# Optimization experiments

Measured on AMD Instinct MI355X. Metric: run time of the kernel, lower is better.

Reference implementation:

```python
import jax, jax.numpy as jnp
import numpy as np

B, S, LEN = 1024, 64, 48          # batch, max atoms, atoms per molecule
N = B * LEN                        # total nodes = node_mask.sum()
E = 4 * N                          # edges (avg degree ~4)
D = 256                            # input_dim == hidden_dim == d_model == d_ff
H, HD = D // 8, 8                  # num_heads = hidden_dim // 8
L = 3                              # transformer layers
VOCAB = 65


def _ln(z, s, b):
    mu = z.mean(-1, keepdims=True)
    var = ((z - mu) ** 2).mean(-1, keepdims=True)
    return (z - mu) * jax.lax.rsqrt(var + 1e-5) * s + b


def _forward(x_atoms, edge_index, node_mask, emb_table, conv1_w, conv1_b,
             conv2_w, conv2_b, in_w, in_b, attn_w, attn_b, proj_w, proj_b,
             ln1_s, ln1_b, ff1_w, ff1_b, ff2_w, ff2_b, ln2_s, ln2_b):
    n = x_atoms.shape[0]
    src, dst = edge_index[0], edge_index[1]
    # Embedding with max_norm=1 (torch renormalizes accessed rows)
    e = emb_table[x_atoms]
    nrm = jnp.linalg.norm(e, axis=-1, keepdims=True)
    e = e * jnp.minimum(1.0, 1.0 / (nrm + 1e-7))
    # GCN symmetric normalization with self-loops (shared by both convs)
    deg = jax.ops.segment_sum(jnp.ones((src.shape[0],), e.dtype), dst, num_segments=n) + 1.0
    dinv = jax.lax.rsqrt(deg)
    coef = (dinv[src] * dinv[dst])[:, None]       # per-edge norm
    self_coef = (dinv * dinv)[:, None]            # self-loop norm

    def gcn(h, W, b):
        h = h @ W
        agg = jax.ops.segment_sum(h[src] * coef, dst, num_segments=n)
        return agg + h * self_coef + b

    ones = jnp.ones((n, 1), e.dtype)
    pe = jax.nn.relu(gcn(ones, conv1_w, conv1_b))
    pe = gcn(pe, conv2_w, conv2_b)
    x = e + pe
    # masked_scatter into padded [B, S, D] (row-major fill order)
    mflat = node_mask.reshape(-1)
    rank = jnp.clip(jnp.cumsum(mflat) - 1, 0, n - 1)
    padded = jnp.where(mflat[:, None], x[rank], 0.0).reshape(B, S, D)
    # transformer encoder, post-LN, ReLU FFN; mask [B,1,S,1] as in original
    h = padded @ in_w + in_b
    qmask = node_mask[:, None, :, None]
    scale = 1.0 / np.sqrt(HD).astype(np.float32)
    for l in range(L):
        qkv = h @ attn_w[l] + attn_b[l]
        q, k, v = jnp.split(qkv, 3, axis=-1)
        q = q.reshape(B, S, H, HD)
        k = k.reshape(B, S, H, HD)
        v = v.reshape(B, S, H, HD)
        scores = jnp.einsum('bqhd,bkhd->bhqk', q, k) * scale
        scores = jnp.where(qmask, scores, -1e9)
        attn = jax.nn.softmax(scores, axis=-1)
        o = jnp.einsum('bhqk,bkhd->bqhd', attn, v).reshape(B, S, D)
        h = _ln(h + o @ proj_w[l] + proj_b[l], ln1_s[l], ln1_b[l])
        ff = jax.nn.relu(h @ ff1_w[l] + ff1_b[l]) @ ff2_w[l] + ff2_b[l]
        h = _ln(h + ff, ln2_s[l], ln2_b[l])
    return h


def setup_inputs() -> dict:
    key = jax.random.key(0)
    ks = jax.random.split(key, 16)
    x_atoms = jax.random.randint(ks[0], (N,), 0, VOCAB)
    edge_index = jax.random.randint(ks[1], (2, E), 0, N)
    node_mask = jnp.broadcast_to(jnp.arange(S)[None, :] < LEN, (B, S))
    f32 = jnp.float32
    p = lambda k, shp: (jax.random.normal(k, shp, f32) * 0.02)
    return {
        'x_atoms': x_atoms, 'edge_index': edge_index, 'node_mask': node_mask,
        'emb_table': jax.random.normal(ks[2], (VOCAB, D), f32),
        'conv1_w': p(ks[3], (1, D)), 'conv1_b': jnp.zeros((D,), f32),
        'conv2_w': p(ks[4], (D, D)), 'conv2_b': jnp.zeros((D,), f32),
        'in_w': p(ks[5], (D, D)), 'in_b': jnp.zeros((D,), f32),
        'attn_w': p(ks[6], (L, D, 3 * D)), 'attn_b': jnp.zeros((L, 3 * D), f32),
        'proj_w': p(ks[7], (L, D, D)), 'proj_b': jnp.zeros((L, D), f32),
        'ln1_s': jnp.ones((L, D), f32), 'ln1_b': jnp.zeros((L, D), f32),
        'ff1_w': p(ks[8], (L, D, D)), 'ff1_b': jnp.zeros((L, D), f32),
        'ff2_w': p(ks[9], (L, D, D)), 'ff2_b': jnp.zeros((L, D), f32),
        'ln2_s': jnp.ones((L, D), f32), 'ln2_b': jnp.zeros((L, D), f32),
    }


def reference(x_atoms, edge_index, node_mask, emb_table, conv1_w, conv1_b,
              conv2_w, conv2_b, in_w, in_b, attn_w, attn_b, proj_w, proj_b,
              ln1_s, ln1_b, ff1_w, ff1_b, ff2_w, ff2_b, ln2_s, ln2_b):
    return _forward(x_atoms, edge_index, node_mask, emb_table, conv1_w, conv1_b,
                    conv2_w, conv2_b, in_w, in_b, attn_w, attn_b, proj_w, proj_b,
                    ln1_s, ln1_b, ff1_w, ff1_b, ff2_w, ff2_b, ln2_s, ln2_b)
```

## Files before the change

### kernel.cpp

```cpp
#include <hip/hip_runtime.h>
#include <cstdint>
#include <cstddef>

#define B_   1024
#define S_   64
#define LEN_ 48
#define NN   (B_*LEN_)
#define EE   (4*NN)
#define D_   256
#define H_   32
#define HD_  8
#define ROWS (B_*S_)
#define PLANE 16777216

typedef float  f32x4  __attribute__((ext_vector_type(4)));
typedef __bf16 bf16x8 __attribute__((ext_vector_type(8)));

#define AS1(p) ((const __attribute__((address_space(1))) void*)(p))
#define AS3(p) ((__attribute__((address_space(3))) void*)(p))

__device__ __forceinline__ unsigned short f2bf(float f) {
    union { float f; unsigned u; } x; x.f = f;
    unsigned r = x.u + 0x7fffu + ((x.u >> 16) & 1u);
    return (unsigned short)(r >> 16);
}
__device__ __forceinline__ float bf2f(unsigned short h) {
    union { unsigned u; float f; } x; x.u = (unsigned)h << 16; return x.f;
}
__device__ __forceinline__ bf16x8 u4_to_bf8(uint4 u) {
    union { uint4 u; bf16x8 v; } c; c.u = u; return c.v;
}

__global__ void embed_kernel(const int* __restrict__ atoms,
                             const float* __restrict__ table,
                             float* __restrict__ e) {
    int wave = threadIdx.x >> 6, lane = threadIdx.x & 63;
    int row  = blockIdx.x * 4 + wave;
    int a    = atoms[row];
    float4 v = ((const float4*)(table + (size_t)a * D_))[lane];
    float ss = v.x*v.x + v.y*v.y + v.z*v.z + v.w*v.w;
    #pragma unroll
    for (int off = 32; off; off >>= 1) ss += __shfl_xor(ss, off);
    float nrm = sqrtf(ss);
    float sc  = fminf(1.0f, 1.0f / (nrm + 1e-7f));
    v.x *= sc; v.y *= sc; v.z *= sc; v.w *= sc;
    ((float4*)(e + (size_t)row * D_))[lane] = v;
}

__global__ void fill_kernel(const int* __restrict__ ei, int* __restrict__ cur,
                            int* __restrict__ bucket) {
    int e = blockIdx.x * 256 + threadIdx.x;
    if (e < EE) {
        int s = ei[e], d = ei[EE + e];
        int pos = atomicAdd(&cur[d], 1);
        if (pos < 32) bucket[d * 32 + pos] = s;
    }
}

__global__ void dinv_kernel(const int* __restrict__ cur, float* __restrict__ dinv) {
    int i = blockIdx.x * 256 + threadIdx.x;
    if (i < NN) dinv[i] = rsqrtf((float)cur[i] + 1.0f);
}

__global__ void agg1_kernel(const int* __restrict__ ei, const float* __restrict__ dinv,
                            float* __restrict__ agg1) {
    int e = blockIdx.x * 256 + threadIdx.x;
    if (e < EE) {
        int s = ei[e], d = ei[EE + e];
        atomicAdd(&agg1[d], dinv[s] * dinv[d]);
    }
}

__global__ void pe1_kernel(const float* __restrict__ agg1, const float* __restrict__ dinv,
                           const float* __restrict__ w1, const float* __restrict__ b1,
                           unsigned short* __restrict__ pe1) {
    size_t idx = (size_t)blockIdx.x * 256 + threadIdx.x;
    int i = (int)(idx >> 8), d = (int)(idx & 255);
    float c = agg1[i] + dinv[i] * dinv[i];
    pe1[idx] = f2bf(fmaxf(0.0f, w1[d] * c + b1[d]));
}

__global__ void wconv_kernel(const float* __restrict__ conv2_w, const float* __restrict__ in_w,
                             const float* __restrict__ attn_w, const float* __restrict__ proj_w,
                             const float* __restrict__ ff1_w, const float* __restrict__ ff2_w,
                             unsigned short* __restrict__ wt) {
    int z = blockIdx.y;
    int n = blockIdx.x, k = threadIdx.x;
    const float* src; unsigned short* dst; int N = 256;
    if      (z == 0) { src = conv2_w;                       dst = wt; }
    else if (z == 1) { src = in_w;                          dst = wt + 65536; }
    else if (z <  5) { int l = z - 2;  src = attn_w + (size_t)l * 196608; dst = wt + 131072  + (size_t)l * 196608; N = 768; }
    else if (z <  8) { int l = z - 5;  src = proj_w + (size_t)l * 65536;  dst = wt + 720896  + (size_t)l * 65536; }
    else if (z < 11) { int l = z - 8;  src = ff1_w  + (size_t)l * 65536;  dst = wt + 917504  + (size_t)l * 65536; }
    else             { int l = z - 11; src = ff2_w  + (size_t)l * 65536;  dst = wt + 1114112 + (size_t)l * 65536; }
    if (n < N) dst[(size_t)n * 256 + k] = f2bf(src[(size_t)k * N + n]);
}

__global__ __launch_bounds__(256) void gemm2(
        const unsigned short* __restrict__ A, const unsigned short* __restrict__ WT,
        const float* __restrict__ bias, unsigned short* __restrict__ C0,
        float* __restrict__ Cf, const unsigned short* __restrict__ zeros,
        int mt, int amode, int cmode, int relu) {
    __shared__ unsigned short sh[16384];
    unsigned short* Asm = sh;
    unsigned short* Wsm = sh + 8192;
    const int t = threadIdx.x, w = t >> 6, lane = t & 63;
    const int lr = lane & 15, lq = lane >> 4;
    const int by = blockIdx.x % mt;
    const int bx = blockIdx.x / mt;
    const size_t m0 = (size_t)by * 128;
    const int    n0 = bx * 128;
    const int    N  = (gridDim.x / mt) * 128;
    const int    wr = (w >> 1) * 64, wc = (w & 1) * 64;

    f32x4 acc[4][4];
    #pragma unroll
    for (int mi = 0; mi < 4; mi++)
        #pragma unroll
        for (int tt = 0; tt < 4; tt++) acc[mi][tt] = (f32x4){0.f, 0.f, 0.f, 0.f};

    const int srow = w * 32 + (lane >> 3);
    const int sj   = lane & 7;

    for (int ki = 0; ki < 4; ki++) {
        if (ki) __syncthreads();
        #pragma unroll
        for (int c = 0; c < 4; c++) {
            int row = srow + c * 8;
            {
                int gch = sj ^ (row & 7);
                const unsigned short* g;
                if (amode == 0) {
                    g = A + (m0 + row) * 256 + ki * 64 + gch * 8;
                } else {
                    size_t grow = m0 + row;
                    int s = (int)(grow & 63);
                    g = (s < LEN_) ? (A + ((grow >> 6) * LEN_ + s) * 256 + ki * 64 + gch * 8)
                                   : zeros;
                }
                __builtin_amdgcn_global_load_lds(AS1(g), AS3(Asm + w * 2048 + c * 512), 16, 0, 0);
            }
            {
                int gch = sj ^ (row & 7);
                const unsigned short* g = WT + (size_t)(n0 + row) * 256 + ki * 64 + gch * 8;
                __builtin_amdgcn_global_load_lds(AS1(g), AS3(Wsm + w * 2048 + c * 512), 16, 0, 0);
            }
        }
        __syncthreads();
        #pragma unroll
        for (int ks = 0; ks < 2; ks++) {
            bf16x8 af[4], bfr[4];
            #pragma unroll
            for (int mi = 0; mi < 4; mi++) {
                int row = wr + mi * 16 + lr;
                int cs = (ks * 4 + lq) ^ (row & 7);
                af[mi] = *(const bf16x8*)&Asm[row * 64 + cs * 8];
            }
            #pragma unroll
            for (int tt = 0; tt < 4; tt++) {
                int col = wc + tt * 16 + lr;
                int cs = (ks * 4 + lq) ^ (col & 7);
                bfr[tt] = *(const bf16x8*)&Wsm[col * 64 + cs * 8];
            }
            #pragma unroll
            for (int mi = 0; mi < 4; mi++)
                #pragma unroll
                for (int tt = 0; tt < 4; tt++)
                    acc[mi][tt] = __builtin_amdgcn_mfma_f32_16x16x32_bf16(af[mi], bfr[tt], acc[mi][tt], 0, 0, 0);
        }
    }
    if (cmode == 2) {
        #pragma unroll
        for (int tt = 0; tt < 4; tt++) {
            int c = n0 + wc + tt * 16 + lr;
            float bv = bias ? bias[c] : 0.0f;
            #pragma unroll
            for (int mi = 0; mi < 4; mi++)
                #pragma unroll
                for (int r = 0; r < 4; r++) {
                    size_t grow = m0 + wr + mi * 16 + lq * 4 + r;
                    float v = acc[mi][tt][r] + bv;
                    C0[grow * 256 + c] = f2bf(v);
                    Cf[grow * 256 + c] = v;
                }
        }
    } else {
        __syncthreads();
        #pragma unroll
        for (int tt = 0; tt < 4; tt++) {
            int col = wc + tt * 16 + lr;
            float bv = bias ? bias[n0 + col] : 0.0f;
            #pragma unroll
            for (int mi = 0; mi < 4; mi++)
                #pragma unroll
                for (int r = 0; r < 4; r++) {
                    int row = wr + mi * 16 + lq * 4 + r;
                    float v = acc[mi][tt][r] + bv;
                    if (relu) v = fmaxf(v, 0.0f);
                    sh[row * 128 + (((col >> 3) ^ (row & 15)) << 3) + (col & 7)] = f2bf(v);
                }
        }
        __syncthreads();
        #pragma unroll
        for (int i = 0; i < 8; i++) {
            int id = i * 256 + t;
            int row = id >> 4, hch = id & 15;
            uint4 val = *(const uint4*)&sh[row * 128 + ((hch ^ (row & 15)) << 3)];
            size_t grow = m0 + row;
            int c0 = n0 + hch * 8;
            if (cmode == 0) {
                *(uint4*)&C0[grow * (size_t)N + c0] = val;
            } else {
                int p = c0 >> 8, h = (c0 >> 3) & 31;
                *(uint4*)&C0[(size_t)p * PLANE + ((grow >> 6) * 32 + h) * 512 + (grow & 63) * 8] = val;
            }
        }
    }
}

__global__ void gather_kernel(const float* __restrict__ xbuf, const unsigned short* __restrict__ h2,
                              const int* __restrict__ cur, const int* __restrict__ bucket,
                              const float* __restrict__ dinv, const float* __restrict__ b2,
                              unsigned short* __restrict__ xg) {
    int w = threadIdx.x >> 6, lane = threadIdx.x & 63;
    int i = blockIdx.x * 4 + w;
    float di = dinv[i];
    ushort4 hv = ((const ushort4*)(h2 + (size_t)i * D_))[lane];
    float4  xv = ((const float4*)(xbuf + (size_t)i * D_))[lane];
    float4  bv = ((const float4*)b2)[lane];
    float a0 = xv.x + bf2f(hv.x) * di * di + bv.x;
    float a1 = xv.y + bf2f(hv.y) * di * di + bv.y;
    float a2 = xv.z + bf2f(hv.z) * di * di + bv.z;
    float a3 = xv.w + bf2f(hv.w) * di * di + bv.w;
    int deg = min(cur[i], 32);
    for (int e = 0; e < deg; e++) {
        int s = bucket[i * 32 + e];
        float c = dinv[s] * di;
        ushort4 sv = ((const ushort4*)(h2 + (size_t)s * D_))[lane];
        a0 += bf2f(sv.x) * c;
        a1 += bf2f(sv.y) * c;
        a2 += bf2f(sv.z) * c;
        a3 += bf2f(sv.w) * c;
    }
    ushort4 out;
    out.x = f2bf(a0); out.y = f2bf(a1); out.z = f2bf(a2); out.w = f2bf(a3);
    ((ushort4*)(xg + (size_t)i * D_))[lane] = out;
}

__global__ __launch_bounds__(256) void attn3_kernel(unsigned short* __restrict__ qkv) {
    __shared__ unsigned short Pb[4][64 * 64];
    __shared__ unsigned short VTb[4][16 * 64];
    const int b = blockIdx.x;
    const int w = threadIdx.x >> 6, lane = threadIdx.x & 63;
    const int lr = lane & 15, lq = lane >> 4;
    unsigned short* Pw  = Pb[w];
    unsigned short* VTw = VTb[w];
    const uint4* Q4 = (const uint4*)qkv;
    const uint4* K4 = Q4 + PLANE / 8;
    const uint4* V4 = Q4 + 2 * (PLANE / 8);
    unsigned short* o = qkv;
    const float scale = 0.35355339059327373f;
    const bf16x8 zf = u4_to_bf8(make_uint4(0, 0, 0, 0));

    for (int hh = 0; hh < 8; hh++) {
        const int h = w * 8 + hh;
        const size_t hb = ((size_t)b * 32 + h) * 64;

        {
            uint4 vrow = V4[hb + lane];
            union { uint4 u; unsigned short s[8]; } vu; vu.u = vrow;
            int ch = lane >> 3, jj = lane & 7;
            #pragma unroll
            for (int d = 0; d < 8; d++)
                VTw[d * 64 + (ch ^ (d & 7)) * 8 + jj] = vu.s[d];
        }

        bf16x8 af[4], bfk[4];
        #pragma unroll
        for (int mi = 0; mi < 4; mi++)
            af[mi] = (lq == 0) ? u4_to_bf8(Q4[hb + mi * 16 + lr]) : zf;
        #pragma unroll
        for (int ni = 0; ni < 4; ni++)
            bfk[ni] = (lq == 0) ? u4_to_bf8(K4[hb + ni * 16 + lr]) : zf;
        f32x4 s[4][4];
        #pragma unroll
        for (int mi = 0; mi < 4; mi++)
            #pragma unroll
            for (int ni = 0; ni < 4; ni++)
                s[mi][ni] = __builtin_amdgcn_mfma_f32_16x16x32_bf16(
                    af[mi], bfk[ni], (f32x4){0.f, 0.f, 0.f, 0.f}, 0, 0, 0);
        #pragma unroll
        for (int ni = 0; ni < 4; ni++) s[3][ni] = (f32x4){0.f, 0.f, 0.f, 0.f};

        #pragma unroll
        for (int mi = 0; mi < 4; mi++) {
            float mx[4], sm[4];
            #pragma unroll
            for (int r = 0; r < 4; r++)
                mx[r] = fmaxf(fmaxf(s[mi][0][r], s[mi][1][r]), fmaxf(s[mi][2][r], s[mi][3][r]));
            #pragma unroll
            for (int st = 1; st <= 8; st <<= 1)
                #pragma unroll
                for (int r = 0; r < 4; r++) mx[r] = fmaxf(mx[r], __shfl_xor(mx[r], st));
            #pragma unroll
            for (int ni = 0; ni < 4; ni++)
                #pragma unroll
                for (int r = 0; r < 4; r++)
                    s[mi][ni][r] = __expf((s[mi][ni][r] - mx[r]) * scale);
            #pragma unroll
            for (int r = 0; r < 4; r++)
                sm[r] = (s[mi][0][r] + s[mi][1][r]) + (s[mi][2][r] + s[mi][3][r]);
            #pragma unroll
            for (int st = 1; st <= 8; st <<= 1)
                #pragma unroll
                for (int r = 0; r < 4; r++) sm[r] += __shfl_xor(sm[r], st);
            #pragma unroll
            for (int r = 0; r < 4; r++) sm[r] = 1.0f / sm[r];
            #pragma unroll
            for (int ni = 0; ni < 4; ni++) {
                int ch = ni * 2 + (lr >> 3), jj = lr & 7;
                #pragma unroll
                for (int r = 0; r < 4; r++) {
                    int q = mi * 16 + lq * 4 + r;
                    Pw[q * 64 + (ch ^ (q & 7)) * 8 + jj] = f2bf(s[mi][ni][r] * sm[r]);
                }
            }
        }

        bf16x8 av[2];
        #pragma unroll
        for (int ks = 0; ks < 2; ks++) {
            int cs = (ks * 4 + lq) ^ (lr & 7);
            av[ks] = *(const bf16x8*)&VTw[lr * 64 + cs * 8];
        }
        #pragma unroll
        for (int ni = 0; ni < 4; ni++) {
            f32x4 oa = (f32x4){0.f, 0.f, 0.f, 0.f};
            #pragma unroll
            for (int ks = 0; ks < 2; ks++) {
                int q = ni * 16 + lr;
                int cs = (ks * 4 + lq) ^ (q & 7);
                bf16x8 pb = *(const bf16x8*)&Pw[q * 64 + cs * 8];
                oa = __builtin_amdgcn_mfma_f32_16x16x32_bf16(av[ks], pb, oa, 0, 0, 0);
            }
            if (lq < 2) {
                int q = ni * 16 + lr;
                ushort4 ov;
                ov.x = f2bf(oa[0]); ov.y = f2bf(oa[1]);
                ov.z = f2bf(oa[2]); ov.w = f2bf(oa[3]);
                *(ushort4*)(o + (hb + q) * 8 + lq * 4) = ov;
            }
        }
    }
}

__global__ __launch_bounds__(256) void projln_kernel(
        const unsigned short* __restrict__ A, const unsigned short* __restrict__ WT,
        const float* __restrict__ bias, const float* __restrict__ resid,
        const float* __restrict__ g, const float* __restrict__ bb,
        float* __restrict__ outF, unsigned short* __restrict__ outB, int aplane) {
    __shared__ unsigned short Asm[64 * 64];
    __shared__ unsigned short Wsm[256 * 64];
    const int t = threadIdx.x, w = t >> 6, lane = t & 63;
    const int lr = lane & 15, lq = lane >> 4;
    const size_t m0 = (size_t)blockIdx.x * 64;
    f32x4 acc[16];
    #pragma unroll
    for (int tt = 0; tt < 16; tt++) acc[tt] = (f32x4){0.f, 0.f, 0.f, 0.f};

    for (int ki = 0; ki < 4; ki++) {
        if (ki) __syncthreads();
        #pragma unroll
        for (int c = 0; c < 2; c++) {
            int rowl = w * 16 + (lane >> 3) + c * 8;
            int gch = (lane & 7) ^ (rowl & 7);
            const unsigned short* gsrc = aplane
                ? A + (((size_t)blockIdx.x * 32 + ki * 8 + gch) * 64 + rowl) * 8
                : A + (m0 + rowl) * 256 + ki * 64 + gch * 8;
            __builtin_amdgcn_global_load_lds(AS1(gsrc), AS3(Asm + w * 1024 + c * 512), 16, 0, 0);
        }
        #pragma unroll
        for (int c = 0; c < 8; c++) {
            int row = w * 64 + (lane >> 3) + c * 8;
            const unsigned short* gsrc = WT + (size_t)row * 256 + ki * 64 + ((lane & 7) ^ (row & 7)) * 8;
            __builtin_amdgcn_global_load_lds(AS1(gsrc), AS3(Wsm + w * 4096 + c * 512), 16, 0, 0);
        }
        __syncthreads();
        #pragma unroll
        for (int ks = 0; ks < 2; ks++) {
            int cs = ((ks * 4 + lq) ^ (lr & 7)) << 3;
            int ra = w * 16 + lr;
            bf16x8 af = *(const bf16x8*)&Asm[ra * 64 + cs];
            #pragma unroll
            for (int tt = 0; tt < 16; tt++) {
                int col = tt * 16 + lr;
                bf16x8 bfr = *(const bf16x8*)&Wsm[col * 64 + cs];
                acc[tt] = __builtin_amdgcn_mfma_f32_16x16x32_bf16(af, bfr, acc[tt], 0, 0, 0);
            }
        }
    }
    float s1[4] = {0.f,0.f,0.f,0.f}, s2[4] = {0.f,0.f,0.f,0.f};
    #pragma unroll
    for (int tt = 0; tt < 16; tt++) {
        int col = tt * 16 + lr;
        float bv = bias[col];
        #pragma unroll
        for (int r = 0; r < 4; r++) {
            size_t grow = m0 + w * 16 + lq * 4 + r;
            float z = acc[tt][r] + bv + resid[grow * 256 + col];
            acc[tt][r] = z;
            s1[r] += z; s2[r] += z * z;
        }
    }
    #pragma unroll
    for (int st = 1; st <= 8; st <<= 1)
        #pragma unroll
        for (int r = 0; r < 4; r++) { s1[r] += __shfl_xor(s1[r], st); s2[r] += __shfl_xor(s2[r], st); }
    float mu[4], rs[4];
    #pragma unroll
    for (int r = 0; r < 4; r++) {
        mu[r] = s1[r] * (1.0f / 256.0f);
        float var = s2[r] * (1.0f / 256.0f) - mu[r] * mu[r];
        rs[r] = rsqrtf(var + 1e-5f);
    }
    #pragma unroll
    for (int tt = 0; tt < 16; tt++) {
        int col = tt * 16 + lr;
        float gv = g[col], bv2 = bb[col];
        #pragma unroll
        for (int r = 0; r < 4; r++) {
            size_t grow = m0 + w * 16 + lq * 4 + r;
            float v = (acc[tt][r] - mu[r]) * rs[r] * gv + bv2;
            outF[grow * 256 + col] = v;
            outB[grow * 256 + col] = f2bf(v);
        }
    }
}

__global__ __launch_bounds__(256) void ffn_kernel(
        const unsigned short* __restrict__ A,
        const unsigned short* __restrict__ W1T, const float* __restrict__ b1,
        const unsigned short* __restrict__ W2T, const float* __restrict__ b2,
        const float* __restrict__ resid,
        const float* __restrict__ g, const float* __restrict__ bb,
        float* __restrict__ outF, unsigned short* __restrict__ outB) {
    __shared__ unsigned short Asm[64 * 32];
    __shared__ unsigned short Wsm[256 * 32];
    __shared__ unsigned short T[64 * 256];
    const int t = threadIdx.x, w = t >> 6, lane = t & 63;
    const int lr = lane & 15, lq = lane >> 4;
    const size_t m0 = (size_t)blockIdx.x * 64;
    f32x4 acc[16];
    #pragma unroll
    for (int tt = 0; tt < 16; tt++) acc[tt] = (f32x4){0.f, 0.f, 0.f, 0.f};

    for (int ki = 0; ki < 8; ki++) {
        if (ki) __syncthreads();
        {
            int rowl = w * 16 + (lane >> 2);
            const unsigned short* gsrc = A + (m0 + rowl) * 256 + ki * 32 + (((lane & 3) ^ (rowl & 3)) << 3);
            __builtin_amdgcn_global_load_lds(AS1(gsrc), AS3(Asm + w * 512), 16, 0, 0);
        }
        #pragma unroll
        for (int c = 0; c < 4; c++) {
            int row = w * 64 + c * 16 + (lane >> 2);
            const unsigned short* gsrc = W1T + (size_t)row * 256 + ki * 32 + (((lane & 3) ^ (row & 3)) << 3);
            __builtin_amdgcn_global_load_lds(AS1(gsrc), AS3(Wsm + w * 2048 + c * 512), 16, 0, 0);
        }
        __syncthreads();
        int cs = (lq ^ (lr & 3)) << 3;
        int ra = w * 16 + lr;
        bf16x8 af = *(const bf16x8*)&Asm[ra * 32 + cs];
        #pragma unroll
        for (int tt = 0; tt < 16; tt++) {
            int col = tt * 16 + lr;
            bf16x8 bfr = *(const bf16x8*)&Wsm[col * 32 + cs];
            acc[tt] = __builtin_amdgcn_mfma_f32_16x16x32_bf16(af, bfr, acc[tt], 0, 0, 0);
        }
    }
    #pragma unroll
    for (int tt = 0; tt < 16; tt++) {
        int col = tt * 16 + lr;
        float bv = b1[col];
        int kig = col >> 5, ch = (col >> 3) & 3, jj = col & 7;
        #pragma unroll
        for (int r = 0; r < 4; r++) {
            int rowl = w * 16 + lq * 4 + r;
            float v = fmaxf(acc[tt][r] + bv, 0.0f);
            int pos = ch ^ (rowl & 3) ^ ((rowl >> 2) & 3);
            T[kig * 2048 + rowl * 32 + pos * 8 + jj] = f2bf(v);
            acc[tt][r] = 0.0f;
        }
    }
    for (int ki = 0; ki < 8; ki++) {
        __syncthreads();
        #pragma unroll
        for (int c = 0; c < 4; c++) {
            int row = w * 64 + c * 16 + (lane >> 2);
            const unsigned short* gsrc = W2T + (size_t)row * 256 + ki * 32 + (((lane & 3) ^ (row & 3)) << 3);
            __builtin_amdgcn_global_load_lds(AS1(gsrc), AS3(Wsm + w * 2048 + c * 512), 16, 0, 0);
        }
        __syncthreads();
        int ra = w * 16 + lr;
        int pos = lq ^ (lr & 3) ^ ((lr >> 2) & 3);
        bf16x8 af = *(const bf16x8*)&T[ki * 2048 + ra * 32 + pos * 8];
        int cs = (lq ^ (lr & 3)) << 3;
        #pragma unroll
        for (int tt = 0; tt < 16; tt++) {
            int col = tt * 16 + lr;
            bf16x8 bfr = *(const bf16x8*)&Wsm[col * 32 + cs];
            acc[tt] = __builtin_amdgcn_mfma_f32_16x16x32_bf16(af, bfr, acc[tt], 0, 0, 0);
        }
    }
    float s1[4] = {0.f,0.f,0.f,0.f}, s2[4] = {0.f,0.f,0.f,0.f};
    #pragma unroll
    for (int tt = 0; tt < 16; tt++) {
        int col = tt * 16 + lr;
        float bv = b2[col];
        #pragma unroll
        for (int r = 0; r < 4; r++) {
            size_t grow = m0 + w * 16 + lq * 4 + r;
            float z = acc[tt][r] + bv + resid[grow * 256 + col];
            acc[tt][r] = z;
            s1[r] += z; s2[r] += z * z;
        }
    }
    #pragma unroll
    for (int st = 1; st <= 8; st <<= 1)
        #pragma unroll
        for (int r = 0; r < 4; r++) { s1[r] += __shfl_xor(s1[r], st); s2[r] += __shfl_xor(s2[r], st); }
    float mu[4], rs[4];
    #pragma unroll
    for (int r = 0; r < 4; r++) {
        mu[r] = s1[r] * (1.0f / 256.0f);
        float var = s2[r] * (1.0f / 256.0f) - mu[r] * mu[r];
        rs[r] = rsqrtf(var + 1e-5f);
    }
    #pragma unroll
    for (int tt = 0; tt < 16; tt++) {
        int col = tt * 16 + lr;
        float gv = g[col], bv2 = bb[col];
        #pragma unroll
        for (int r = 0; r < 4; r++) {
            size_t grow = m0 + w * 16 + lq * 4 + r;
            float v = (acc[tt][r] - mu[r]) * rs[r] * gv + bv2;
            outF[grow * 256 + col] = v;
            if (outB) outB[grow * 256 + col] = f2bf(v);
        }
    }
}

extern "C" void kernel_launch(void* const* d_in, const int* in_sizes, int n_in,
                              void* d_out, int out_size, void* d_ws, size_t ws_size,
                              hipStream_t stream) {
    const int*   x_atoms = (const int*)d_in[0];
    const int*   ei      = (const int*)d_in[1];
    const float* emb     = (const float*)d_in[3];
    const float* conv1_w = (const float*)d_in[4];
    const float* conv1_b = (const float*)d_in[5];
    const float* conv2_w = (const float*)d_in[6];
    const float* conv2_b = (const float*)d_in[7];
    const float* in_w    = (const float*)d_in[8];
    const float* in_b    = (const float*)d_in[9];
    const float* attn_w  = (const float*)d_in[10];
    const float* attn_b  = (const float*)d_in[11];
    const float* proj_w  = (const float*)d_in[12];
    const float* proj_b  = (const float*)d_in[13];
    const float* ln1_s   = (const float*)d_in[14];
    const float* ln1_b   = (const float*)d_in[15];
    const float* ff1_w   = (const float*)d_in[16];
    const float* ff1_b   = (const float*)d_in[17];
    const float* ff2_w   = (const float*)d_in[18];
    const float* ff2_b   = (const float*)d_in[19];
    const float* ln2_s   = (const float*)d_in[20];
    const float* ln2_b   = (const float*)d_in[21];

    char* ws = (char*)d_ws;
    float*          xbuf = (float*)         (ws + 0);
    unsigned short* pe1  = (unsigned short*)(ws + 50331648);
    unsigned short* xg   = (unsigned short*)(ws + 50331648);
    unsigned short* h2   = (unsigned short*)(ws + 75497472);
    unsigned short* Qp   = (unsigned short*)(ws + 0);
    float*          hbuf = (float*)         (ws + 100663296);
    unsigned short* hbf  = (unsigned short*)(ws + 167772160);
    int*            bucket=(int*)           (ws + 201326592);
    unsigned short* wt   = (unsigned short*)(ws + 207618048);
    int*            cur  = (int*)           (ws + 210239488);
    float*          dinv = (float*)         (ws + 210436096);
    float*          agg1 = (float*)         (ws + 210632704);
    unsigned short* zpage= (unsigned short*)(ws + 210829312);

    hipMemsetAsync(cur,   0, NN * 4, stream);
    hipMemsetAsync(agg1,  0, NN * 4, stream);
    hipMemsetAsync(zpage, 0, 256, stream);

    wconv_kernel<<<dim3(768, 14), 256, 0, stream>>>(conv2_w, in_w, attn_w, proj_w, ff1_w, ff2_w, wt);

    embed_kernel<<<NN / 4, 256, 0, stream>>>(x_atoms, emb, xbuf);
    fill_kernel<<<EE / 256, 256, 0, stream>>>(ei, cur, bucket);
    dinv_kernel<<<NN / 256, 256, 0, stream>>>(cur, dinv);
    agg1_kernel<<<EE / 256, 256, 0, stream>>>(ei, dinv, agg1);
    pe1_kernel<<<NN, 256, 0, stream>>>(agg1, dinv, conv1_w, conv1_b, pe1);
    gemm2<<<768, 256, 0, stream>>>(pe1, wt, nullptr, h2, nullptr, zpage, 384, 0, 0, 0);
    gather_kernel<<<NN / 4, 256, 0, stream>>>(xbuf, h2, cur, bucket, dinv, conv2_b, xg);

    gemm2<<<1024, 256, 0, stream>>>(xg, wt + 65536, in_b, hbf, hbuf, zpage, 512, 1, 2, 0);

    for (int l = 0; l < 3; l++) {
        gemm2<<<3072, 256, 0, stream>>>(
            hbf, wt + 131072 + (size_t)l * 196608, attn_b + (size_t)l * 768,
            Qp, nullptr, zpage, 512, 0, 3, 0);
        attn3_kernel<<<B_, 256, 0, stream>>>(Qp);
        projln_kernel<<<ROWS / 64, 256, 0, stream>>>(
            Qp, wt + 720896 + (size_t)l * 65536, proj_b + (size_t)l * D_, hbuf,
            ln1_s + (size_t)l * D_, ln1_b + (size_t)l * D_, hbuf, hbf, 1);
        ffn_kernel<<<ROWS / 64, 256, 0, stream>>>(
            hbf, wt + 917504 + (size_t)l * 65536, ff1_b + (size_t)l * D_,
            wt + 1114112 + (size_t)l * 65536, ff2_b + (size_t)l * D_, hbuf,
            ln2_s + (size_t)l * D_, ln2_b + (size_t)l * D_,
            (l == 2) ? (float*)d_out : hbuf, (l == 2) ? nullptr : hbf);
    }
}
```

Baseline: 1.048 ms.

## Remap GEMM blocks across XCDs and widen FFN K-steps with register-held A

The generic GEMM now maps block indices so that consecutive blocks on the same XCD share the same weight column tile across M rows, aiming for better L2 locality on the multi-die GPU. The fused FFN kernel keeps the A fragment in registers, loaded once from global memory, instead of staging it through LDS. It also doubles the K chunk per iteration to 64 with an 8-way XOR swizzle, halving the number of barrier and load rounds. The trade-off is more registers per thread and a larger LDS footprint, which may lower occupancy. The XCD mapping also assumes the M-tile count is divisible by 8.

```diff
diff --git a/kernel.cpp b/kernel.cpp
--- a/kernel.cpp
+++ b/kernel.cpp
@@ -106,11 +106,14 @@
     unsigned short* Wsm = sh + 8192;
     const int t = threadIdx.x, w = t >> 6, lane = t & 63;
     const int lr = lane & 15, lq = lane >> 4;
-    const int by = blockIdx.x % mt;
-    const int bx = blockIdx.x / mt;
+    const int nt = gridDim.x / mt;
+    const int xcd = blockIdx.x & 7;
+    const int sb  = blockIdx.x >> 3;
+    const int bx = sb % nt;
+    const int by = (sb / nt) * 8 + xcd;
     const size_t m0 = (size_t)by * 128;
     const int    n0 = bx * 128;
-    const int    N  = (gridDim.x / mt) * 128;
+    const int    N  = nt * 128;
     const int    wr = (w >> 1) * 64, wc = (w & 1) * 64;
 
     f32x4 acc[4][4];
@@ -444,72 +447,81 @@
         const float* __restrict__ resid,
         const float* __restrict__ g, const float* __restrict__ bb,
         float* __restrict__ outF, unsigned short* __restrict__ outB) {
-    __shared__ unsigned short Asm[64 * 32];
-    __shared__ unsigned short Wsm[256 * 32];
+    __shared__ unsigned short Wsm[256 * 64];
     __shared__ unsigned short T[64 * 256];
     const int t = threadIdx.x, w = t >> 6, lane = t & 63;
     const int lr = lane & 15, lq = lane >> 4;
     const size_t m0 = (size_t)blockIdx.x * 64;
+
+    uint4 afu[8];
+    {
+        const unsigned short* arow = A + (m0 + w * 16 + lr) * 256 + lq * 8;
+        #pragma unroll
+        for (int s = 0; s < 8; s++) afu[s] = *(const uint4*)(arow + s * 32);
+    }
     f32x4 acc[16];
     #pragma unroll
     for (int tt = 0; tt < 16; tt++) acc[tt] = (f32x4){0.f, 0.f, 0.f, 0.f};
 
-    for (int ki = 0; ki < 8; ki++) {
+    for (int ki = 0; ki < 4; ki++) {
         if (ki) __syncthreads();
-        {
-            int rowl = w * 16 + (lane >> 2);
-            const unsigned short* gsrc = A + (m0 + rowl) * 256 + ki * 32 + (((lane & 3) ^ (rowl & 3)) << 3);
-            __builtin_amdgcn_global_load_lds(AS1(gsrc), AS3(Asm + w * 512), 16, 0, 0);
-        }
-        #pragma unroll
-        for (int c = 0; c < 4; c++) {
-            int row = w * 64 + c * 16 + (lane >> 2);
-            const unsigned short* gsrc = W1T + (size_t)row * 256 + ki * 32 + (((lane & 3) ^ (row & 3)) << 3);
-            __builtin_amdgcn_global_load_lds(AS1(gsrc), AS3(Wsm + w * 2048 + c * 512), 16, 0, 0);
+        #pragma unroll
+        for (int i = 0; i < 8; i++) {
+            int id = i * 256 + t;
+            int row = id >> 3, c = id & 7;
+            const unsigned short* src = W1T + (size_t)row * 256 + ki * 64 + ((c ^ (row & 7)) << 3);
+            __builtin_amdgcn_global_load_lds(AS1(src), AS3(Wsm + id * 8), 16, 0, 0);
         }
         __syncthreads();
-        int cs = (lq ^ (lr & 3)) << 3;
-        int ra = w * 16 + lr;
-        bf16x8 af = *(const bf16x8*)&Asm[ra * 32 + cs];
-        #pragma unroll
-        for (int tt = 0; tt < 16; tt++) {
-            int col = tt * 16 + lr;
-            bf16x8 bfr = *(const bf16x8*)&Wsm[col * 32 + cs];
-            acc[tt] = __builtin_amdgcn_mfma_f32_16x16x32_bf16(af, bfr, acc[tt], 0, 0, 0);
+        #pragma unroll
+        for (int ks = 0; ks < 2; ks++) {
+            bf16x8 af = u4_to_bf8(afu[ki * 2 + ks]);
+            #pragma unroll
+            for (int tt = 0; tt < 16; tt++) {
+                int row = tt * 16 + lr;
+                int pos = (ks * 4 + lq) ^ (row & 7);
+                bf16x8 bfr = *(const bf16x8*)&Wsm[row * 64 + pos * 8];
+                acc[tt] = __builtin_amdgcn_mfma_f32_16x16x32_bf16(af, bfr, acc[tt], 0, 0, 0);
+            }
         }
     }
     #pragma unroll
     for (int tt = 0; tt < 16; tt++) {
-        int col = tt * 16 + lr;
-        float bv = b1[col];
-        int kig = col >> 5, ch = (col >> 3) & 3, jj = col & 7;
+        int ff = tt * 16 + lr;
+        float bv = b1[ff];
+        int chunk = ff >> 3, jj = ff & 7;
         #pragma unroll
         for (int r = 0; r < 4; r++) {
-            int rowl = w * 16 + lq * 4 + r;
+            int m = w * 16 + lq * 4 + r;
             float v = fmaxf(acc[tt][r] + bv, 0.0f);
-            int pos = ch ^ (rowl & 3) ^ ((rowl >> 2) & 3);
-            T[kig * 2048 + rowl * 32 + pos * 8 + jj] = f2bf(v);
+            int pos = chunk ^ (m & 7) ^ ((m >> 3) & 3);
+            T[m * 256 + pos * 8 + jj] = f2bf(v);
             acc[tt][r] = 0.0f;
         }
     }
-    for (int ki = 0; ki < 8; ki++) {
+    for (int ki = 0; ki < 4; ki++) {
         __syncthreads();
         #pragma unroll
-        for (int c = 0; c < 4; c++) {
-            int row = w * 64 + c * 16 + (lane >> 2);
-            const unsigned short* gsrc = W2T + (size_t)row * 256 + ki * 32 + (((lane & 3) ^ (row & 3)) << 3);
-            __builtin_amdgcn_global_load_lds(AS1(gsrc), AS3(Wsm + w * 2048 + c * 512), 16, 0, 0);
+        for (int i = 0; i < 8; i++) {
+            int id = i * 256 + t;
+            int row = id >> 3, c = id & 7;
+            const unsigned short* src = W2T + (size_t)row * 256 + ki * 64 + ((c ^ (row & 7)) << 3);
+            __builtin_amdgcn_global_load_lds(AS1(src), AS3(Wsm + id * 8), 16, 0, 0);
         }
         __syncthreads();
-        int ra = w * 16 + lr;
-        int pos = lq ^ (lr & 3) ^ ((lr >> 2) & 3);
-        bf16x8 af = *(const bf16x8*)&T[ki * 2048 + ra * 32 + pos * 8];
-        int cs = (lq ^ (lr & 3)) << 3;
-        #pragma unroll
-        for (int tt = 0; tt < 16; tt++) {
-            int col = tt * 16 + lr;
-            bf16x8 bfr = *(const bf16x8*)&Wsm[col * 32 + cs];
-            acc[tt] = __builtin_amdgcn_mfma_f32_16x16x32_bf16(af, bfr, acc[tt], 0, 0, 0);
+        #pragma unroll
+        for (int ks = 0; ks < 2; ks++) {
+            int m = w * 16 + lr;
+            int chunk = (ki * 2 + ks) * 4 + lq;
+            int pos = chunk ^ (m & 7) ^ ((m >> 3) & 3);
+            bf16x8 af = *(const bf16x8*)&T[m * 256 + pos * 8];
+            #pragma unroll
+            for (int tt = 0; tt < 16; tt++) {
+                int row = tt * 16 + lr;
+                int wpos = (ks * 4 + lq) ^ (row & 7);
+                bf16x8 bfr = *(const bf16x8*)&Wsm[row * 64 + wpos * 8];
+                acc[tt] = __builtin_amdgcn_mfma_f32_16x16x32_bf16(af, bfr, acc[tt], 0, 0, 0);
+            }
         }
     }
     float s1[4] = {0.f,0.f,0.f,0.f}, s2[4] = {0.f,0.f,0.f,0.f};
```

After: 1.001 ms. 1.05x faster.
